# Kernel optimization log

Measured on AMD Instinct MI355X. Metric: run time of the kernel, lower is better.

## Reference

```python
import jax, jax.numpy as jnp
import numpy as np

N = 8000      # nodes
E = 64000     # edges
IN = 16       # node feature dim
H = 128       # hidden_dim
M = 16        # msg_dim
ED = 4        # edge feature dim
OUT = 4       # targets
L = 2         # num_layers
EPS = 1e-5    # batchnorm eps


def setup_inputs() -> dict:
    key = jax.random.key(0)
    ks = jax.random.split(key, 16)
    s = 0.05
    return {
        "x": jax.random.normal(ks[0], (N, IN), jnp.float32),
        "edge_index": jax.random.randint(ks[1], (2, E), 0, N),
        "edge_attr": jax.random.normal(ks[2], (E, ED), jnp.float32),
        # input projection
        "in_W": jax.random.normal(ks[3], (IN, H), jnp.float32) * s,
        "in_b": jnp.zeros((H,), jnp.float32),
        # per-layer NNConv edge MLP: Linear(ED,H) -> ReLU -> Linear(H, M*H)
        "conv_W1": jax.random.normal(ks[4], (L, ED, H), jnp.float32) * s,
        "conv_b1": jnp.zeros((L, H), jnp.float32),
        "conv_W2": jax.random.normal(ks[5], (L, H, M * H), jnp.float32) * s,
        "conv_b2": jnp.zeros((L, M * H), jnp.float32),
        # NNConv root weight and bias (root_weight=True, bias=True defaults)
        "root_W": jax.random.normal(ks[6], (L, H, M), jnp.float32) * s,
        "conv_bias": jnp.zeros((L, M), jnp.float32),
        # batchnorm affine params
        "bn_gamma": jnp.ones((L, H), jnp.float32),
        "bn_beta": jnp.zeros((L, H), jnp.float32),
        # msg_proj: Linear(M, H)
        "msg_W": jax.random.normal(ks[7], (L, M, H), jnp.float32) * s,
        "msg_b": jnp.zeros((L, H), jnp.float32),
        # output projection
        "out_W": jax.random.normal(ks[8], (H, OUT), jnp.float32) * s,
        "out_b": jnp.zeros((OUT,), jnp.float32),
    }


def reference(x, edge_index, edge_attr, in_W, in_b, conv_W1, conv_b1,
              conv_W2, conv_b2, root_W, conv_bias, bn_gamma, bn_beta,
              msg_W, msg_b, out_W, out_b):
    src, dst = edge_index[0], edge_index[1]
    # in-degree for mean aggregation (clamped to avoid div-by-zero)
    deg = jax.ops.segment_sum(jnp.ones((E,), x.dtype), dst, num_segments=N)
    deg = jnp.maximum(deg, 1.0)[:, None]                       # [N,1]

    h = x @ in_W + in_b                                        # [N,H]
    for l in range(L):
        # edge NN -> per-edge weight matrices [E,H,M]
        We = jax.nn.relu(edge_attr @ conv_W1[l] + conv_b1[l])  # [E,H]
        We = (We @ conv_W2[l] + conv_b2[l]).reshape(E, H, M)
        # per-edge matvec on source node features, scatter-mean to targets
        msgs = jnp.einsum('eh,ehm->em', h[src], We)            # [E,M]
        agg = jax.ops.segment_sum(msgs, dst, num_segments=N) / deg  # [N,M]
        x_msg = agg + h @ root_W[l] + conv_bias[l]             # [N,M]
        # residual + msg projection
        h = h + x_msg @ msg_W[l] + msg_b[l]                    # [N,H]
        # batchnorm (batch statistics, biased var, as in torch training fwd)
        mu = h.mean(axis=0)
        var = jnp.mean((h - mu) ** 2, axis=0)
        h = bn_gamma[l] * (h - mu) * jax.lax.rsqrt(var + EPS) + bn_beta[l]
        h = jax.nn.relu(h)
        # dropout p=0.0 -> identity
    return h @ out_W + out_b                                   # [N,OUT]
```

## Files before the change

### kernel.cpp

```cpp
#include <hip/hip_runtime.h>

#define NN 8000
#define NE 64000
#define INF 16
#define HH 128
#define MM 16
#define EDF 4
#define OUTF 4
#define NL 2
#define BN_EPS 1e-5f
#define BPR 2080
#define CAP 48
#define QS 2052

typedef __attribute__((ext_vector_type(8))) short short8;
typedef __attribute__((ext_vector_type(4))) float f32x4;

static __device__ __forceinline__ unsigned short f2bf(float f) {
  unsigned u = __builtin_bit_cast(unsigned, f);
  u = (u + 0x7fffu + ((u >> 16) & 1u)) >> 16;
  return (unsigned short)u;
}
static __device__ __forceinline__ float bf2f(unsigned short s) {
  unsigned u = ((unsigned)s) << 16;
  return __builtin_bit_cast(float, u);
}
static __device__ __forceinline__ int qperm(int k) {
  return ((k >> 3) & 3) | ((k & 7) << 2) | (k & 0x60);
}

__global__ __launch_bounds__(128) void front_k(
    const float* __restrict__ x, const float* __restrict__ inW,
    const float* __restrict__ inb, const int* __restrict__ ei,
    const float* __restrict__ ea,
    const float* __restrict__ W2, const float* __restrict__ b2,
    const float* __restrict__ rW,
    unsigned short* __restrict__ hb,
    float* __restrict__ deg, int* __restrict__ cnt,
    unsigned short* __restrict__ Bp, float* __restrict__ agg,
    float* __restrict__ ea_s, int* __restrict__ dst_s) {
  int blk = blockIdx.x;
  int t = threadIdx.x;
  __shared__ float sx[INF];
  if (t < INF) sx[t] = x[blk * INF + t];
  __syncthreads();
  float acc = inb[t];
#pragma unroll
  for (int i = 0; i < INF; ++i) acc = fmaf(sx[i], inW[i * HH + t], acc);
  hb[(size_t)blk * HH + t] = f2bf(acc);

  if (blk < 500) {
    int e = blk * 128 + t;
    int src = ei[e], dst = ei[NE + e];
    atomicAdd(&deg[dst], 1.0f);
    int slot = atomicAdd(&cnt[src], 1);
    int p = src * CAP + slot;
    *(float4*)&ea_s[(size_t)p * 4] = *(const float4*)&ea[(size_t)e * 4];
    dst_s[p] = dst;
  } else if (blk < 756) {
    int r = blk - 500;
    int l = r >> 7, k = r & 127;
    const float* w2row = W2 + (size_t)l * (HH * HH * MM) + (size_t)k * 2048;
    float4 v0 = *(const float4*)&w2row[t * 16 + 0];
    float4 v1 = *(const float4*)&w2row[t * 16 + 4];
    float4 v2 = *(const float4*)&w2row[t * 16 + 8];
    float4 v3 = *(const float4*)&w2row[t * 16 + 12];
    unsigned short* bpr = Bp + ((size_t)l * BPR + (size_t)k * 16) * HH + t;
#pragma unroll
    for (int j = 0; j < 4; ++j) bpr[(0 + j) * HH] = f2bf((&v0.x)[j]);
#pragma unroll
    for (int j = 0; j < 4; ++j) bpr[(4 + j) * HH] = f2bf((&v1.x)[j]);
#pragma unroll
    for (int j = 0; j < 4; ++j) bpr[(8 + j) * HH] = f2bf((&v2.x)[j]);
#pragma unroll
    for (int j = 0; j < 4; ++j) bpr[(12 + j) * HH] = f2bf((&v3.x)[j]);
  } else if (blk < 760) {
    int isroot = (blk >= 758);
    int l = (blk - 756) & 1;
    const float* src = isroot ? (rW + (size_t)l * HH * MM) : (b2 + (size_t)l * 2048);
    float4 v0 = *(const float4*)&src[t * 16 + 0];
    float4 v1 = *(const float4*)&src[t * 16 + 4];
    float4 v2 = *(const float4*)&src[t * 16 + 8];
    float4 v3 = *(const float4*)&src[t * 16 + 12];
    unsigned short* bpr = Bp + ((size_t)l * BPR + 2048 + isroot * 16) * HH + t;
#pragma unroll
    for (int j = 0; j < 4; ++j) bpr[(0 + j) * HH] = f2bf((&v0.x)[j]);
#pragma unroll
    for (int j = 0; j < 4; ++j) bpr[(4 + j) * HH] = f2bf((&v1.x)[j]);
#pragma unroll
    for (int j = 0; j < 4; ++j) bpr[(8 + j) * HH] = f2bf((&v2.x)[j]);
#pragma unroll
    for (int j = 0; j < 4; ++j) bpr[(12 + j) * HH] = f2bf((&v3.x)[j]);
  } else if (blk < 885) {
    int i = (blk - 760) * 256 + t;
    uint4 z = make_uint4(0, 0, 0, 0);
    ((uint4*)agg)[i] = z;
    ((uint4*)agg)[i + 128] = z;
  }
}

__global__ __launch_bounds__(1024) void fused_layer_k(
    const unsigned short* __restrict__ hb, const float* __restrict__ hpre,
    const float* __restrict__ bnsums, const float* __restrict__ gamma,
    const float* __restrict__ beta, int bn_mode,
    const unsigned short* __restrict__ Bp,
    const float* __restrict__ ea_s, const int* __restrict__ dst_s,
    const int* __restrict__ cnt, const float* __restrict__ W1,
    const float* __restrict__ b1, float* __restrict__ agg,
    float* __restrict__ Xroot) {
  __shared__ unsigned short sA[2 * 16 * 136];
  __shared__ unsigned short sQ[2 * 16 * QS];
  __shared__ float sW1[EDF * HH];
  __shared__ float sb1[HH];
  __shared__ float sB2[32][17];
  __shared__ float sscl[HH], sshf[HH];

  int tid = threadIdx.x;
  int n0 = blockIdx.x * 32;
  int wid = tid >> 6, lane = tid & 63;
  int l15 = lane & 15, l4 = lane >> 4;

  for (int i = tid; i < EDF * HH; i += 1024) sW1[i] = W1[i];
  if (tid < HH) sb1[tid] = b1[tid];
  if (bn_mode && tid >= 128 && tid < 256) {
    int c = tid - 128;
    float mu = bnsums[c] * (1.0f / NN);
    float var = bnsums[HH + c] * (1.0f / NN) - mu * mu;
    float sc = gamma[c] * rsqrtf(var + BN_EPS);
    sscl[c] = sc;
    sshf[c] = beta[c] - mu * sc;
  }
  __syncthreads();

  if (tid < 512) {
    int g = tid >> 8;
    int node = (tid >> 4) & 15;
    int c0 = (tid & 15) * 8;
    int ng = n0 + g * 16 + node;
    if (bn_mode == 0) {
      uint4 v = *(const uint4*)&hb[(size_t)ng * HH + c0];
      *(uint4*)&sA[g * 2176 + node * 136 + c0] = v;
    } else {
      float4 v0 = *(const float4*)&hpre[(size_t)ng * HH + c0];
      float4 v1 = *(const float4*)&hpre[(size_t)ng * HH + c0 + 4];
      short8 o;
#pragma unroll
      for (int j = 0; j < 4; ++j) {
        o[j] = (short)f2bf(fmaxf(0.f, fmaf((&v0.x)[j], sscl[c0 + j], sshf[c0 + j])));
        o[4 + j] = (short)f2bf(fmaxf(0.f, fmaf((&v1.x)[j], sscl[c0 + 4 + j], sshf[c0 + 4 + j])));
      }
      *(short8*)&sA[g * 2176 + node * 136 + c0] = o;
    }
  }
  __syncthreads();

  short8 A0 = *(const short8*)&sA[l15 * 136 + 0 * 32 + l4 * 8];
  short8 A1 = *(const short8*)&sA[l15 * 136 + 1 * 32 + l4 * 8];
  short8 A2 = *(const short8*)&sA[l15 * 136 + 2 * 32 + l4 * 8];
  short8 A3 = *(const short8*)&sA[l15 * 136 + 3 * 32 + l4 * 8];
  short8 A4 = *(const short8*)&sA[2176 + l15 * 136 + 0 * 32 + l4 * 8];
  short8 A5 = *(const short8*)&sA[2176 + l15 * 136 + 1 * 32 + l4 * 8];
  short8 A6 = *(const short8*)&sA[2176 + l15 * 136 + 2 * 32 + l4 * 8];
  short8 A7 = *(const short8*)&sA[2176 + l15 * 136 + 3 * 32 + l4 * 8];

  int ctb = wid * 8;
  for (int ct = ctb; ct < ctb + 8; ++ct) {
    const unsigned short* p_ = Bp + ((size_t)(ct * 16 + l15)) * HH + l4 * 8;
    short8 b0 = *(const short8*)(p_);
    short8 b1v = *(const short8*)(p_ + 32);
    short8 b2v_ = *(const short8*)(p_ + 64);
    short8 b3 = *(const short8*)(p_ + 96);
    f32x4 pa = {0.f, 0.f, 0.f, 0.f};
    f32x4 qa = {0.f, 0.f, 0.f, 0.f};
    pa = __builtin_amdgcn_mfma_f32_16x16x32_bf16(A0, b0, pa, 0, 0, 0);
    pa = __builtin_amdgcn_mfma_f32_16x16x32_bf16(A1, b1v, pa, 0, 0, 0);
    pa = __builtin_amdgcn_mfma_f32_16x16x32_bf16(A2, b2v_, pa, 0, 0, 0);
    pa = __builtin_amdgcn_mfma_f32_16x16x32_bf16(A3, b3, pa, 0, 0, 0);
    qa = __builtin_amdgcn_mfma_f32_16x16x32_bf16(A4, b0, qa, 0, 0, 0);
    qa = __builtin_amdgcn_mfma_f32_16x16x32_bf16(A5, b1v, qa, 0, 0, 0);
    qa = __builtin_amdgcn_mfma_f32_16x16x32_bf16(A6, b2v_, qa, 0, 0, 0);
    qa = __builtin_amdgcn_mfma_f32_16x16x32_bf16(A7, b3, qa, 0, 0, 0);
    int kq = qperm(ct) * 16 + l15;
#pragma unroll
    for (int j = 0; j < 4; ++j) {
      sQ[(l4 * 4 + j) * QS + kq] = f2bf(pa[j]);
      sQ[16 * QS + (l4 * 4 + j) * QS + kq] = f2bf(qa[j]);
    }
  }

  if (wid >= 14) {
    int base = (wid == 14) ? 2048 : 2064;
    const unsigned short* p = Bp + ((size_t)(base + l15)) * HH + l4 * 8;
    short8 c0 = *(const short8*)(p);
    short8 c1 = *(const short8*)(p + 32);
    short8 c2 = *(const short8*)(p + 64);
    short8 c3 = *(const short8*)(p + 96);
    f32x4 pa = {0.f, 0.f, 0.f, 0.f};
    f32x4 qa = {0.f, 0.f, 0.f, 0.f};
    pa = __builtin_amdgcn_mfma_f32_16x16x32_bf16(A0, c0, pa, 0, 0, 0);
    pa = __builtin_amdgcn_mfma_f32_16x16x32_bf16(A1, c1, pa, 0, 0, 0);
    pa = __builtin_amdgcn_mfma_f32_16x16x32_bf16(A2, c2, pa, 0, 0, 0);
    pa = __builtin_amdgcn_mfma_f32_16x16x32_bf16(A3, c3, pa, 0, 0, 0);
    qa = __builtin_amdgcn_mfma_f32_16x16x32_bf16(A4, c0, qa, 0, 0, 0);
    qa = __builtin_amdgcn_mfma_f32_16x16x32_bf16(A5, c1, qa, 0, 0, 0);
    qa = __builtin_amdgcn_mfma_f32_16x16x32_bf16(A6, c2, qa, 0, 0, 0);
    qa = __builtin_amdgcn_mfma_f32_16x16x32_bf16(A7, c3, qa, 0, 0, 0);
    if (wid == 14) {
#pragma unroll
      for (int j = 0; j < 4; ++j) {
        sB2[l4 * 4 + j][l15] = pa[j];
        sB2[16 + l4 * 4 + j][l15] = qa[j];
      }
    } else {
#pragma unroll
      for (int j = 0; j < 4; ++j) {
        Xroot[(size_t)(n0 + l4 * 4 + j) * MM + l15] = pa[j];
        Xroot[(size_t)(n0 + 16 + l4 * 4 + j) * MM + l15] = qa[j];
      }
    }
  }
  __syncthreads();

  for (int gi = 0; gi < 2; ++gi) {
    int nl = gi * 16 + wid;
    int n = n0 + nl;
    int count = cnt[n];
    if (count == 0) continue;

    const unsigned short* sq = &sQ[gi * 16 * QS + (nl & 15) * QS];
    short8 qb0, qb1, qb2, qb3;
#pragma unroll
    for (int j = 0; j < 8; ++j) {
      qb0[j] = (short)sq[qperm(0 * 32 + l4 * 8 + j) * 16 + l15];
      qb1[j] = (short)sq[qperm(1 * 32 + l4 * 8 + j) * 16 + l15];
      qb2[j] = (short)sq[qperm(2 * 32 + l4 * 8 + j) * 16 + l15];
      qb3[j] = (short)sq[qperm(3 * 32 + l4 * 8 + j) * 16 + l15];
    }
    float b2v = sB2[nl][l15];

    const float* eab = ea_s + (size_t)n * CAP * 4;
    const int* dsb = dst_s + (size_t)n * CAP;
    for (int t0 = 0; t0 < count; t0 += 16) {
      int rr = t0 + l15;
      bool valid = rr < count;
      float4 eav = valid ? *(const float4*)&eab[(size_t)rr * 4]
                         : make_float4(0.f, 0.f, 0.f, 0.f);
      f32x4 acc = {0.f, 0.f, 0.f, 0.f};
#pragma unroll
      for (int ks = 0; ks < 4; ++ks) {
        short8 a;
#pragma unroll
        for (int j = 0; j < 8; ++j) {
          int k = ks * 32 + l4 * 8 + j;
          float r = fmaf(eav.w, sW1[3 * HH + k],
                     fmaf(eav.z, sW1[2 * HH + k],
                       fmaf(eav.y, sW1[HH + k], fmaf(eav.x, sW1[k], sb1[k]))));
          a[j] = valid ? (short)f2bf(fmaxf(r, 0.f)) : (short)0;
        }
        short8 qb = (ks == 0) ? qb0 : (ks == 1) ? qb1 : (ks == 2) ? qb2 : qb3;
        acc = __builtin_amdgcn_mfma_f32_16x16x32_bf16(a, qb, acc, 0, 0, 0);
      }
#pragma unroll
      for (int j = 0; j < 4; ++j) {
        int r = t0 + l4 * 4 + j;
        if (r < count) {
          atomicAdd(&agg[(size_t)dsb[r] * MM + l15], acc[j] + b2v);
        }
      }
    }
  }
}

__global__ __launch_bounds__(256) void node_update_k(
    const unsigned short* __restrict__ hb, const float* __restrict__ hsrc_pre,
    const float* __restrict__ bnsums, const float* __restrict__ gamma,
    const float* __restrict__ beta, int bn_mode,
    float* __restrict__ agg, const float* __restrict__ deg,
    const float* __restrict__ Xroot, const float* __restrict__ cbias,
    const float* __restrict__ msgW, const float* __restrict__ msgb,
    float* __restrict__ hpre, float* __restrict__ sums) {
  __shared__ float smw[MM * HH];
  __shared__ float xm[16][MM];
  __shared__ float scb[MM];
  __shared__ float smb[HH];
  __shared__ float red[256];
  __shared__ float sscl[HH], sshf[HH];
  int tid = threadIdx.x;
  int n0 = blockIdx.x * 16;
  for (int i = tid; i < MM * HH; i += 256) smw[i] = msgW[i];
  if (tid < MM) scb[tid] = cbias[tid];
  if (tid < HH) smb[tid] = msgb[tid];
  if (bn_mode && tid < HH) {
    float mu = bnsums[tid] * (1.0f / NN);
    float var = bnsums[HH + tid] * (1.0f / NN) - mu * mu;
    float sc = gamma[tid] * rsqrtf(var + BN_EPS);
    sscl[tid] = sc;
    sshf[tid] = beta[tid] - mu * sc;
  }
  __syncthreads();

  {
    int ni = tid >> 4, m = tid & 15;
    int n = n0 + ni;
    size_t idx = (size_t)n * MM + m;
    xm[ni][m] = agg[idx] / fmaxf(deg[n], 1.0f) + Xroot[idx] + scb[m];
  }
  __syncthreads();
  agg[(size_t)n0 * MM + tid] = 0.f;

  int t = tid & 127;
  float lsum = 0.f, lss = 0.f;
#pragma unroll
  for (int pass = 0; pass < 8; ++pass) {
    int ni = pass * 2 + (tid >> 7);
    size_t idx = (size_t)(n0 + ni) * HH + t;
    float resid;
    if (bn_mode) {
      resid = fmaxf(0.f, fmaf(hsrc_pre[idx], sscl[t], sshf[t]));
    } else {
      resid = bf2f(hb[idx]);
    }
    float hp = resid + smb[t];
#pragma unroll
    for (int m = 0; m < MM; ++m) hp = fmaf(xm[ni][m], smw[m * HH + t], hp);
    hpre[idx] = hp;
    lsum += hp;
    lss = fmaf(hp, hp, lss);
  }
  red[tid] = lsum;
  __syncthreads();
  if (tid < 128) atomicAdd(&sums[t], red[tid] + red[tid + 128]);
  __syncthreads();
  red[tid] = lss;
  __syncthreads();
  if (tid < 128) atomicAdd(&sums[HH + t], red[tid] + red[tid + 128]);
}

__global__ void out_proj_k(const float* __restrict__ hpre,
                           const float* __restrict__ bnsums,
                           const float* __restrict__ gamma,
                           const float* __restrict__ beta,
                           const float* __restrict__ W, const float* __restrict__ b,
                           float* __restrict__ out) {
  __shared__ float sscl[HH], sshf[HH];
  int tid = threadIdx.x;
  if (tid < HH) {
    float mu = bnsums[tid] * (1.0f / NN);
    float var = bnsums[HH + tid] * (1.0f / NN) - mu * mu;
    float sc = gamma[tid] * rsqrtf(var + BN_EPS);
    sscl[tid] = sc;
    sshf[tid] = beta[tid] - mu * sc;
  }
  __syncthreads();
  int n = blockIdx.x * 4 + (tid >> 6);
  int lane = tid & 63;
  if (n >= NN) return;
  float acc0 = 0.f, acc1 = 0.f, acc2 = 0.f, acc3 = 0.f;
#pragma unroll
  for (int rep = 0; rep < 2; ++rep) {
    int hh = lane + rep * 64;
    float hv = fmaxf(0.f, fmaf(hpre[(size_t)n * HH + hh], sscl[hh], sshf[hh]));
    acc0 = fmaf(hv, W[hh * OUTF + 0], acc0);
    acc1 = fmaf(hv, W[hh * OUTF + 1], acc1);
    acc2 = fmaf(hv, W[hh * OUTF + 2], acc2);
    acc3 = fmaf(hv, W[hh * OUTF + 3], acc3);
  }
#pragma unroll
  for (int s = 32; s > 0; s >>= 1) {
    acc0 += __shfl_down(acc0, s);
    acc1 += __shfl_down(acc1, s);
    acc2 += __shfl_down(acc2, s);
    acc3 += __shfl_down(acc3, s);
  }
  if (lane == 0) {
    out[n * OUTF + 0] = acc0 + b[0];
    out[n * OUTF + 1] = acc1 + b[1];
    out[n * OUTF + 2] = acc2 + b[2];
    out[n * OUTF + 3] = acc3 + b[3];
  }
}

extern "C" void kernel_launch(void* const* d_in, const int* in_sizes, int n_in,
                              void* d_out, int out_size, void* d_ws, size_t ws_size,
                              hipStream_t stream) {
  (void)in_sizes; (void)n_in; (void)out_size; (void)ws_size;
  const float* x    = (const float*)d_in[0];
  const int* ei     = (const int*)d_in[1];
  const float* ea   = (const float*)d_in[2];
  const float* inW  = (const float*)d_in[3];
  const float* inb  = (const float*)d_in[4];
  const float* cW1  = (const float*)d_in[5];
  const float* cb1  = (const float*)d_in[6];
  const float* cW2  = (const float*)d_in[7];
  const float* cb2  = (const float*)d_in[8];
  const float* rW   = (const float*)d_in[9];
  const float* cbias= (const float*)d_in[10];
  const float* gam  = (const float*)d_in[11];
  const float* bet  = (const float*)d_in[12];
  const float* mW   = (const float*)d_in[13];
  const float* mb   = (const float*)d_in[14];
  const float* oW   = (const float*)d_in[15];
  const float* ob   = (const float*)d_in[16];
  float* out = (float*)d_out;

  float* ws = (float*)d_ws;
  size_t off = 0;
  float* deg   = ws + off; off += 8192;
  int* cnt     = (int*)(ws + off); off += 8192;
  float* sums0 = ws + off; off += 256;
  float* sums1 = ws + off; off += 256;
  size_t zero_floats = off;
  float* agg   = ws + off; off += (size_t)NN * MM;
  float* hpre0 = ws + off; off += (size_t)NN * HH;
  float* hpre1 = ws + off; off += (size_t)NN * HH;
  float* Xroot = ws + off; off += (size_t)NN * MM;
  unsigned short* hb = (unsigned short*)(ws + off); off += (size_t)NN * HH / 2;
  unsigned short* Bp = (unsigned short*)(ws + off); off += (size_t)NL * BPR * HH / 2;
  float* ea_s  = ws + off; off += (size_t)NN * CAP * 4;
  int* dst_s   = (int*)(ws + off); off += (size_t)NN * CAP;

  hipMemsetAsync(deg, 0, zero_floats * sizeof(float), stream);
  front_k<<<NN, 128, 0, stream>>>(x, inW, inb, ei, ea, cW2, cb2, rW, hb,
                                  deg, cnt, Bp, agg, ea_s, dst_s);

  fused_layer_k<<<NN / 32, 1024, 0, stream>>>(hb, hpre0, sums0, gam, bet, 0,
                                              Bp, ea_s, dst_s, cnt, cW1, cb1,
                                              agg, Xroot);
  node_update_k<<<NN / 16, 256, 0, stream>>>(hb, hpre0, sums0, gam, bet, 0,
                                             agg, deg, Xroot, cbias, mW, mb,
                                             hpre0, sums0);
  fused_layer_k<<<NN / 32, 1024, 0, stream>>>(hb, hpre0, sums0, gam, bet, 1,
                                              Bp + (size_t)BPR * HH, ea_s, dst_s,
                                              cnt, cW1 + EDF * HH, cb1 + HH,
                                              agg, Xroot);
  node_update_k<<<NN / 16, 256, 0, stream>>>(hb, hpre0, sums0, gam, bet, 1,
                                             agg, deg, Xroot, cbias + MM,
                                             mW + MM * HH, mb + HH,
                                             hpre1, sums1);
  out_proj_k<<<NN / 4, 256, 0, stream>>>(hpre1, sums1, gam + HH, bet + HH,
                                         oW, ob, out);
}
```

Measured before the change: 121.0 us.

## Fuse input projection into layer kernel and halve nodes per block

The input projection x@inW moves out of the front kernel, which now launches only the blocks needed for edge bucketing and weight packing. The first fused layer instead computes h for its nodes directly into shared memory, reusing the sQ buffer as scratch, and also writes it to global memory. Each fused-layer block now handles 16 nodes instead of 32, which doubles the grid and halves shared memory per block so occupancy can rise. In exchange, every block reloads Bp and recomputes the shared-weight MFMAs with half the reuse, and each block stages all of inW.

```diff
diff --git a/kernel.cpp b/kernel.cpp
--- a/kernel.cpp
+++ b/kernel.cpp
@@ -30,24 +30,14 @@
 }
 
 __global__ __launch_bounds__(128) void front_k(
-    const float* __restrict__ x, const float* __restrict__ inW,
-    const float* __restrict__ inb, const int* __restrict__ ei,
-    const float* __restrict__ ea,
+    const int* __restrict__ ei, const float* __restrict__ ea,
     const float* __restrict__ W2, const float* __restrict__ b2,
     const float* __restrict__ rW,
-    unsigned short* __restrict__ hb,
     float* __restrict__ deg, int* __restrict__ cnt,
     unsigned short* __restrict__ Bp, float* __restrict__ agg,
     float* __restrict__ ea_s, int* __restrict__ dst_s) {
   int blk = blockIdx.x;
   int t = threadIdx.x;
-  __shared__ float sx[INF];
-  if (t < INF) sx[t] = x[blk * INF + t];
-  __syncthreads();
-  float acc = inb[t];
-#pragma unroll
-  for (int i = 0; i < INF; ++i) acc = fmaf(sx[i], inW[i * HH + t], acc);
-  hb[(size_t)blk * HH + t] = f2bf(acc);
 
   if (blk < 500) {
     int e = blk * 128 + t;
@@ -99,8 +89,10 @@
   }
 }
 
-__global__ __launch_bounds__(1024) void fused_layer_k(
-    const unsigned short* __restrict__ hb, const float* __restrict__ hpre,
+__global__ __launch_bounds__(1024, 8) void fused_layer_k(
+    const float* __restrict__ x, const float* __restrict__ inW,
+    const float* __restrict__ inb, unsigned short* __restrict__ hb,
+    const float* __restrict__ hpre,
     const float* __restrict__ bnsums, const float* __restrict__ gamma,
     const float* __restrict__ beta, int bn_mode,
     const unsigned short* __restrict__ Bp,
@@ -108,49 +100,68 @@
     const int* __restrict__ cnt, const float* __restrict__ W1,
     const float* __restrict__ b1, float* __restrict__ agg,
     float* __restrict__ Xroot) {
-  __shared__ unsigned short sA[2 * 16 * 136];
-  __shared__ unsigned short sQ[2 * 16 * QS];
+  __shared__ unsigned short sA[16 * 136];
+  __shared__ unsigned short sQ[16 * QS];
   __shared__ float sW1[EDF * HH];
   __shared__ float sb1[HH];
-  __shared__ float sB2[32][17];
+  __shared__ float sB2[16][17];
   __shared__ float sscl[HH], sshf[HH];
 
+  float* sIW = (float*)sQ;
+  float* sX = (float*)(sQ + 4096);
+
   int tid = threadIdx.x;
-  int n0 = blockIdx.x * 32;
+  int n0 = blockIdx.x * 16;
   int wid = tid >> 6, lane = tid & 63;
   int l15 = lane & 15, l4 = lane >> 4;
 
   for (int i = tid; i < EDF * HH; i += 1024) sW1[i] = W1[i];
   if (tid < HH) sb1[tid] = b1[tid];
-  if (bn_mode && tid >= 128 && tid < 256) {
-    int c = tid - 128;
-    float mu = bnsums[c] * (1.0f / NN);
-    float var = bnsums[HH + c] * (1.0f / NN) - mu * mu;
-    float sc = gamma[c] * rsqrtf(var + BN_EPS);
-    sscl[c] = sc;
-    sshf[c] = beta[c] - mu * sc;
-  }
-  __syncthreads();
-
-  if (tid < 512) {
-    int g = tid >> 8;
-    int node = (tid >> 4) & 15;
+  if (bn_mode) {
+    if (tid >= 128 && tid < 256) {
+      int c = tid - 128;
+      float mu = bnsums[c] * (1.0f / NN);
+      float var = bnsums[HH + c] * (1.0f / NN) - mu * mu;
+      float sc = gamma[c] * rsqrtf(var + BN_EPS);
+      sscl[c] = sc;
+      sshf[c] = beta[c] - mu * sc;
+    }
+  } else {
+    if (tid >= 256 && tid < 512) sX[tid - 256] = x[(size_t)n0 * INF + (tid - 256)];
+    if (tid >= 768 && tid < 896) sscl[tid - 768] = inb[tid - 768];
+    for (int i = tid; i < INF * HH; i += 1024) sIW[i] = inW[i];
+  }
+  __syncthreads();
+
+  if (bn_mode == 0) {
+    if (tid < 512) {
+      int nl = tid >> 5;
+      int c0 = (tid & 31) * 4;
+      ushort4 o;
+#pragma unroll
+      for (int j = 0; j < 4; ++j) {
+        int c = c0 + j;
+        float acc = sscl[c];
+#pragma unroll
+        for (int i = 0; i < INF; ++i) acc = fmaf(sX[nl * INF + i], sIW[i * HH + c], acc);
+        (&o.x)[j] = f2bf(acc);
+      }
+      *(ushort4*)&sA[nl * 136 + c0] = o;
+      *(ushort4*)&hb[(size_t)(n0 + nl) * HH + c0] = o;
+    }
+  } else if (tid < 256) {
+    int node = tid >> 4;
     int c0 = (tid & 15) * 8;
-    int ng = n0 + g * 16 + node;
-    if (bn_mode == 0) {
-      uint4 v = *(const uint4*)&hb[(size_t)ng * HH + c0];
-      *(uint4*)&sA[g * 2176 + node * 136 + c0] = v;
-    } else {
-      float4 v0 = *(const float4*)&hpre[(size_t)ng * HH + c0];
-      float4 v1 = *(const float4*)&hpre[(size_t)ng * HH + c0 + 4];
-      short8 o;
-#pragma unroll
-      for (int j = 0; j < 4; ++j) {
-        o[j] = (short)f2bf(fmaxf(0.f, fmaf((&v0.x)[j], sscl[c0 + j], sshf[c0 + j])));
-        o[4 + j] = (short)f2bf(fmaxf(0.f, fmaf((&v1.x)[j], sscl[c0 + 4 + j], sshf[c0 + 4 + j])));
-      }
-      *(short8*)&sA[g * 2176 + node * 136 + c0] = o;
-    }
+    int ng = n0 + node;
+    float4 v0 = *(const float4*)&hpre[(size_t)ng * HH + c0];
+    float4 v1 = *(const float4*)&hpre[(size_t)ng * HH + c0 + 4];
+    short8 o;
+#pragma unroll
+    for (int j = 0; j < 4; ++j) {
+      o[j] = (short)f2bf(fmaxf(0.f, fmaf((&v0.x)[j], sscl[c0 + j], sshf[c0 + j])));
+      o[4 + j] = (short)f2bf(fmaxf(0.f, fmaf((&v1.x)[j], sscl[c0 + 4 + j], sshf[c0 + 4 + j])));
+    }
+    *(short8*)&sA[node * 136 + c0] = o;
   }
   __syncthreads();
 
@@ -158,10 +169,6 @@
   short8 A1 = *(const short8*)&sA[l15 * 136 + 1 * 32 + l4 * 8];
   short8 A2 = *(const short8*)&sA[l15 * 136 + 2 * 32 + l4 * 8];
   short8 A3 = *(const short8*)&sA[l15 * 136 + 3 * 32 + l4 * 8];
-  short8 A4 = *(const short8*)&sA[2176 + l15 * 136 + 0 * 32 + l4 * 8];
-  short8 A5 = *(const short8*)&sA[2176 + l15 * 136 + 1 * 32 + l4 * 8];
-  short8 A6 = *(const short8*)&sA[2176 + l15 * 136 + 2 * 32 + l4 * 8];
-  short8 A7 = *(const short8*)&sA[2176 + l15 * 136 + 3 * 32 + l4 * 8];
 
   int ctb = wid * 8;
   for (int ct = ctb; ct < ctb + 8; ++ct) {
@@ -171,21 +178,15 @@
     short8 b2v_ = *(const short8*)(p_ + 64);
     short8 b3 = *(const short8*)(p_ + 96);
     f32x4 pa = {0.f, 0.f, 0.f, 0.f};
-    f32x4 qa = {0.f, 0.f, 0.f, 0.f};
     pa = __builtin_amdgcn_mfma_f32_16x16x32_bf16(A0, b0, pa, 0, 0, 0);
     pa = __builtin_amdgcn_mfma_f32_16x16x32_bf16(A1, b1v, pa, 0, 0, 0);
     pa = __builtin_amdgcn_mfma_f32_16x16x32_bf16(A2, b2v_, pa, 0, 0, 0);
     pa = __builtin_amdgcn_mfma_f32_16x16x32_bf16(A3, b3, pa, 0, 0, 0);
-    qa = __builtin_amdgcn_mfma_f32_16x16x32_bf16(A4, b0, qa, 0, 0, 0);
-    qa = __builtin_amdgcn_mfma_f32_16x16x32_bf16(A5, b1v, qa, 0, 0, 0);
-    qa = __builtin_amdgcn_mfma_f32_16x16x32_bf16(A6, b2v_, qa, 0, 0, 0);
-    qa = __builtin_amdgcn_mfma_f32_16x16x32_bf16(A7, b3, qa, 0, 0, 0);
     int kq = qperm(ct) * 16 + l15;
-#pragma unroll
-    for (int j = 0; j < 4; ++j) {
-      sQ[(l4 * 4 + j) * QS + kq] = f2bf(pa[j]);
-      sQ[16 * QS + (l4 * 4 + j) * QS + kq] = f2bf(qa[j]);
-    }
+    sQ[(l4 * 4 + 0) * QS + kq] = f2bf(pa[0]);
+    sQ[(l4 * 4 + 1) * QS + kq] = f2bf(pa[1]);
+    sQ[(l4 * 4 + 2) * QS + kq] = f2bf(pa[2]);
+    sQ[(l4 * 4 + 3) * QS + kq] = f2bf(pa[3]);
   }
 
   if (wid >= 14) {
@@ -196,38 +197,28 @@
     short8 c2 = *(const short8*)(p + 64);
     short8 c3 = *(const short8*)(p + 96);
     f32x4 pa = {0.f, 0.f, 0.f, 0.f};
-    f32x4 qa = {0.f, 0.f, 0.f, 0.f};
     pa = __builtin_amdgcn_mfma_f32_16x16x32_bf16(A0, c0, pa, 0, 0, 0);
     pa = __builtin_amdgcn_mfma_f32_16x16x32_bf16(A1, c1, pa, 0, 0, 0);
     pa = __builtin_amdgcn_mfma_f32_16x16x32_bf16(A2, c2, pa, 0, 0, 0);
     pa = __builtin_amdgcn_mfma_f32_16x16x32_bf16(A3, c3, pa, 0, 0, 0);
-    qa = __builtin_amdgcn_mfma_f32_16x16x32_bf16(A4, c0, qa, 0, 0, 0);
-    qa = __builtin_amdgcn_mfma_f32_16x16x32_bf16(A5, c1, qa, 0, 0, 0);
-    qa = __builtin_amdgcn_mfma_f32_16x16x32_bf16(A6, c2, qa, 0, 0, 0);
-    qa = __builtin_amdgcn_mfma_f32_16x16x32_bf16(A7, c3, qa, 0, 0, 0);
     if (wid == 14) {
 #pragma unroll
-      for (int j = 0; j < 4; ++j) {
-        sB2[l4 * 4 + j][l15] = pa[j];
-        sB2[16 + l4 * 4 + j][l15] = qa[j];
-      }
+      for (int j = 0; j < 4; ++j) sB2[l4 * 4 + j][l15] = pa[j];
     } else {
 #pragma unroll
-      for (int j = 0; j < 4; ++j) {
+      for (int j = 0; j < 4; ++j)
         Xroot[(size_t)(n0 + l4 * 4 + j) * MM + l15] = pa[j];
-        Xroot[(size_t)(n0 + 16 + l4 * 4 + j) * MM + l15] = qa[j];
-      }
-    }
-  }
-  __syncthreads();
-
-  for (int gi = 0; gi < 2; ++gi) {
-    int nl = gi * 16 + wid;
+    }
+  }
+  __syncthreads();
+
+  {
+    int nl = wid;
     int n = n0 + nl;
     int count = cnt[n];
-    if (count == 0) continue;
-
-    const unsigned short* sq = &sQ[gi * 16 * QS + (nl & 15) * QS];
+    if (count == 0) return;
+
+    const unsigned short* sq = &sQ[nl * QS];
     short8 qb0, qb1, qb2, qb3;
 #pragma unroll
     for (int j = 0; j < 8; ++j) {
@@ -420,16 +411,18 @@
   int* dst_s   = (int*)(ws + off); off += (size_t)NN * CAP;
 
   hipMemsetAsync(deg, 0, zero_floats * sizeof(float), stream);
-  front_k<<<NN, 128, 0, stream>>>(x, inW, inb, ei, ea, cW2, cb2, rW, hb,
-                                  deg, cnt, Bp, agg, ea_s, dst_s);
-
-  fused_layer_k<<<NN / 32, 1024, 0, stream>>>(hb, hpre0, sums0, gam, bet, 0,
+  front_k<<<885, 128, 0, stream>>>(ei, ea, cW2, cb2, rW, deg, cnt, Bp, agg,
+                                   ea_s, dst_s);
+
+  fused_layer_k<<<NN / 16, 1024, 0, stream>>>(x, inW, inb, hb, hpre0,
+                                              sums0, gam, bet, 0,
                                               Bp, ea_s, dst_s, cnt, cW1, cb1,
                                               agg, Xroot);
   node_update_k<<<NN / 16, 256, 0, stream>>>(hb, hpre0, sums0, gam, bet, 0,
                                              agg, deg, Xroot, cbias, mW, mb,
                                              hpre0, sums0);
-  fused_layer_k<<<NN / 32, 1024, 0, stream>>>(hb, hpre0, sums0, gam, bet, 1,
+  fused_layer_k<<<NN / 16, 1024, 0, stream>>>(x, inW, inb, hb, hpre0,
+                                              sums0, gam, bet, 1,
                                               Bp + (size_t)BPR * HH, ea_s, dst_s,
                                               cnt, cW1 + EDF * HH, cb1 + HH,
                                               agg, Xroot);
```

After: 136.5 us. 12.8% more time.
